# Performance work log

Measured on AMD Instinct MI355X. Metric: run time of the kernel, lower is better.

## Reference

```python
import jax, jax.numpy as jnp
import numpy as np

N_NODES = 50000
N_EDGES = 1600000
DIM = 128
EDGE_DIM = 16
IN_DIM = 2 * DIM + EDGE_DIM


def setup_inputs() -> dict:
    key = jax.random.key(0)
    ks = jax.random.split(key, 8)
    h = jax.random.normal(ks[0], (N_NODES, DIM), dtype=jnp.float32)
    src = jax.random.randint(ks[1], (N_EDGES,), 0, N_NODES)
    dst = jax.random.randint(ks[2], (N_EDGES,), 0, N_NODES)
    edge_attr = jax.random.normal(ks[3], (N_EDGES, EDGE_DIM), dtype=jnp.float32)
    # Linear weights stored as [in, out] so x @ W + b
    W1 = jax.random.normal(ks[4], (IN_DIM, DIM), dtype=jnp.float32) / np.sqrt(IN_DIM)
    b1 = jnp.zeros((DIM,), dtype=jnp.float32)
    W2 = jax.random.normal(ks[5], (DIM, DIM), dtype=jnp.float32) / np.sqrt(DIM)
    b2 = jnp.zeros((DIM,), dtype=jnp.float32)
    gamma = jnp.ones((DIM,), dtype=jnp.float32)
    beta = jnp.zeros((DIM,), dtype=jnp.float32)
    return {"h": h, "src": src, "dst": dst, "edge_attr": edge_attr,
            "W1": W1, "b1": b1, "W2": W2, "b2": b2, "gamma": gamma, "beta": beta}


def _layer_norm(x, gamma, beta, eps=1e-5):
    mu = jnp.mean(x, axis=-1, keepdims=True)
    var = jnp.mean(jnp.square(x - mu), axis=-1, keepdims=True)
    return (x - mu) * jax.lax.rsqrt(var + eps) * gamma + beta


def reference(h, src, dst, edge_attr, W1, b1, W2, b2, gamma, beta):
    # gather endpoint features + edge attrs -> [E, 2*dim+edge_dim]
    x = jnp.concatenate([h[src], h[dst], edge_attr], axis=-1)
    hdn = jax.nn.gelu(x @ W1 + b1, approximate=False)  # torch nn.GELU default is exact
    messages = hdn @ W2 + b2                           # [E, dim]
    # scatter-add messages to destination nodes
    agg = jax.ops.segment_sum(messages, dst, num_segments=h.shape[0])
    return _layer_norm(h + agg, gamma, beta)
```

## Files before the change

kernel.cpp:

```cpp
#include <hip/hip_runtime.h>
#include <math.h>

#define NUM_NODES 50000
#define NUM_EDGES 1600000
#define DIM 128
#define EDGE_DIM 16
#define NKT1 18
#define NKT2 8
#define MT 64
#define CSTRIDE 132
#define NSCAN 196
#define NODE_BLOCKS ((NUM_NODES + 63) / 64)

typedef short bf16x8 __attribute__((ext_vector_type(8)));
typedef float floatx16 __attribute__((ext_vector_type(16)));
typedef unsigned short ushort4v __attribute__((ext_vector_type(4)));
typedef unsigned short ushort8v __attribute__((ext_vector_type(8)));

__device__ __forceinline__ unsigned short f2b(float f) {
    unsigned u = __builtin_bit_cast(unsigned, f);
    u += 0x7FFFu + ((u >> 16) & 1u);
    return (unsigned short)(u >> 16);
}

__global__ void setup_kernel(const float* __restrict__ W1, const float* __restrict__ W2,
                             short* __restrict__ W1f, short* __restrict__ W2f,
                             const float* __restrict__ h, unsigned short* __restrict__ h_bf,
                             const int* __restrict__ dst, int* __restrict__ counts)
{
    int b = blockIdx.x, tid = threadIdx.x;
    if (b < 26) {
        int gid = b * 256 + tid;
        if (gid < NKT1 * 4 * 64) {
            int lane = gid & 63, nb = (gid >> 6) & 3, kt = gid >> 8;
            int n = nb * 32 + (lane & 31);
            int kbase = kt * 16 + (lane >> 5) * 8;
            #pragma unroll
            for (int j = 0; j < 8; ++j) {
                int k = kbase + j;
                W1f[gid * 8 + j] = (k < 272) ? (short)f2b(W1[(size_t)k * DIM + n]) : (short)0;
            }
        } else if (gid < NKT1 * 4 * 64 + NKT2 * 4 * 64) {
            int g2 = gid - NKT1 * 4 * 64;
            int lane = g2 & 63, nb = (g2 >> 6) & 3, kt = g2 >> 8;
            int n = nb * 32 + (lane & 31);
            int kbase = kt * 16 + (lane >> 5) * 8;
            #pragma unroll
            for (int j = 0; j < 8; ++j)
                W2f[g2 * 8 + j] = (short)f2b(W2[(size_t)(kbase + j) * DIM + n]);
        }
    } else if (b < 6276) {
        int t = (b - 26) * 256 + tid;
        float4 v = ((const float4*)h)[t];
        ushort4v o;
        o.x = f2b(v.x); o.y = f2b(v.y); o.z = f2b(v.z); o.w = f2b(v.w);
        ((ushort4v*)h_bf)[t] = o;
    } else {
        int e = (b - 6276) * 256 + tid;
        atomicAdd(&counts[dst[e]], 1);
    }
}

__global__ void scanA_kernel(const int* __restrict__ counts, int* __restrict__ bsum) {
    __shared__ int sb[256];
    int t = threadIdx.x, i = blockIdx.x * 256 + t;
    int v = (i < NUM_NODES) ? counts[i] : 0;
    sb[t] = v; __syncthreads();
    for (int off = 1; off < 256; off <<= 1) {
        int x = (t >= off) ? sb[t - off] : 0;
        __syncthreads(); sb[t] += x; __syncthreads();
    }
    if (t == 255) bsum[blockIdx.x] = sb[255];
}

__global__ void scanB_kernel(const int* __restrict__ bsum, int* __restrict__ boffs) {
    __shared__ int sb[256];
    int t = threadIdx.x;
    int v = (t < NSCAN) ? bsum[t] : 0;
    sb[t] = v; __syncthreads();
    for (int off = 1; off < 256; off <<= 1) {
        int x = (t >= off) ? sb[t - off] : 0;
        __syncthreads(); sb[t] += x; __syncthreads();
    }
    if (t < NSCAN) boffs[t] = sb[t] - v;
}

__global__ void scanC_kernel(const int* __restrict__ counts, const int* __restrict__ boffs,
                             int* __restrict__ cursor) {
    __shared__ int sb[256];
    int t = threadIdx.x, i = blockIdx.x * 256 + t;
    int v = (i < NUM_NODES) ? counts[i] : 0;
    sb[t] = v; __syncthreads();
    for (int off = 1; off < 256; off <<= 1) {
        int x = (t >= off) ? sb[t - off] : 0;
        __syncthreads(); sb[t] += x; __syncthreads();
    }
    if (i < NUM_NODES) cursor[i] = boffs[blockIdx.x] + sb[t] - v;
}

__global__ void scatter_kernel(const int* __restrict__ src, const int* __restrict__ dst,
                               int* __restrict__ cursor, int2* __restrict__ se_s)
{
    int e = blockIdx.x * 256 + threadIdx.x;
    int d = dst[e];
    int p = atomicAdd(&cursor[d], 1);
    se_s[p] = make_int2(src[e] | (d << 16), e);
}

__global__ __launch_bounds__(256, 4) void edge_kernel(
    const unsigned short* __restrict__ h_bf,
    const int2* __restrict__ se_s, const float* __restrict__ ea,
    const short* __restrict__ W1f, const float* __restrict__ pb1,
    float* __restrict__ aggh)
{
    __shared__ __align__(16) short xbuf[36 * 64 * 8];
    __shared__ int dstl[MT];
    float* cbuf = (float*)xbuf;
    float* pbuf = (float*)xbuf;

    const int tid = threadIdx.x;
    const int lane = tid & 63, wave = tid >> 6;
    const long long base = (long long)blockIdx.x * MT;

    {
        int row = lane;
        int2 se = se_s[base + row];
        int sn = se.x & 0xFFFF;
        int dn = ((unsigned)se.x) >> 16;
        if (tid < MT) dstl[tid] = dn;
        const ushort8v* hs = (const ushort8v*)(h_bf + (size_t)sn * DIM);
        const ushort8v* hd = (const ushort8v*)(h_bf + (size_t)dn * DIM);
        #pragma unroll
        for (int it = 0; it < 4; ++it) {
            int kt2 = it * 4 + wave;
            *(ushort8v*)&xbuf[(kt2 * 64 + row) * 8] = hs[kt2];
        }
        #pragma unroll
        for (int it = 0; it < 4; ++it) {
            int kt2 = it * 4 + wave;
            *(ushort8v*)&xbuf[((16 + kt2) * 64 + row) * 8] = hd[kt2];
        }
        if (tid < 128) {
            int r2 = tid >> 1, hc = tid & 1;
            int eid = se_s[base + r2].y;
            const float4* er = (const float4*)(ea + (size_t)eid * EDGE_DIM + hc * 8);
            float4 v0 = er[0], v1 = er[1];
            ushort8v o;
            o[0] = f2b(v0.x); o[1] = f2b(v0.y); o[2] = f2b(v0.z); o[3] = f2b(v0.w);
            o[4] = f2b(v1.x); o[5] = f2b(v1.y); o[6] = f2b(v1.z); o[7] = f2b(v1.w);
            *(ushort8v*)&xbuf[((32 + hc) * 64 + r2) * 8] = o;
        } else {
            int t2 = tid - 128;
            int r2 = t2 >> 1, hc = t2 & 1;
            ushort8v z = {0, 0, 0, 0, 0, 0, 0, 0};
            *(ushort8v*)&xbuf[((34 + hc) * 64 + r2) * 8] = z;
        }
    }
    __syncthreads();

    const int lm = lane & 31, half = lane >> 5;

    floatx16 acc0 = {}, acc1 = {};
    #pragma unroll
    for (int kt = 0; kt < NKT1; ++kt) {
        bf16x8 a0 = *(const bf16x8*)&xbuf[((kt * 2 + half) * 64 + lm) * 8];
        bf16x8 a1 = *(const bf16x8*)&xbuf[((kt * 2 + half) * 64 + 32 + lm) * 8];
        bf16x8 b  = *(const bf16x8*)(W1f + ((kt * 4 + wave) * 64 + lane) * 8);
        acc0 = __builtin_amdgcn_mfma_f32_32x32x16_bf16(a0, b, acc0, 0, 0, 0);
        acc1 = __builtin_amdgcn_mfma_f32_32x32x16_bf16(a1, b, acc1, 0, 0, 0);
    }
    __syncthreads();

    {
        float bb = pb1[wave * 32 + lm];
        #pragma unroll
        for (int s = 0; s < 2; ++s) {
            const floatx16& A = s ? acc1 : acc0;
            #pragma unroll
            for (int r = 0; r < 16; ++r) {
                int rr = (r & 3) + 8 * (r >> 2) + 4 * half;
                float v = A[r] + bb;
                float u = v * (1.5957691216f + 0.0713548163f * v * v);
                u = fminf(u, 80.f);
                float t = __expf(u);
                float g = v * t * __builtin_amdgcn_rcpf(t + 1.f);
                cbuf[(s * 32 + rr) * CSTRIDE + wave * 32 + lm] = g;
            }
        }
    }
    __syncthreads();

    int q = tid & 31, g = tid >> 5;
    float4 s4;
    {
        int r0 = g * 8;
        float4 v[8];
        #pragma unroll
        for (int r = 0; r < 8; ++r)
            v[r] = *(const float4*)&cbuf[(r0 + r) * CSTRIDE + q * 4];
        int d[8];
        #pragma unroll
        for (int r = 0; r < 8; ++r) d[r] = dstl[r0 + r];
        s4 = make_float4(0.f, 0.f, 0.f, 0.f);
        int cur = d[0];
        #pragma unroll
        for (int r = 0; r < 8; ++r) {
            s4.x += v[r].x; s4.y += v[r].y; s4.z += v[r].z; s4.w += v[r].w;
            if (r < 7 && d[r + 1] != cur) {
                float* ap = &aggh[(size_t)cur * DIM + q * 4];
                atomicAdd(ap + 0, s4.x); atomicAdd(ap + 1, s4.y);
                atomicAdd(ap + 2, s4.z); atomicAdd(ap + 3, s4.w);
                s4 = make_float4(0.f, 0.f, 0.f, 0.f);
                cur = d[r + 1];
            }
        }
    }
    __syncthreads();
    *(float4*)&pbuf[g * CSTRIDE + q * 4] = s4;
    __syncthreads();

    if (tid < 128) {
        int col = tid;
        float p[8];
        #pragma unroll
        for (int gg = 0; gg < 8; ++gg) p[gg] = pbuf[gg * CSTRIDE + col];
        int t[8];
        #pragma unroll
        for (int gg = 0; gg < 8; ++gg) t[gg] = dstl[gg * 8 + 7];
        float s = 0.f;
        int cur = t[0];
        #pragma unroll
        for (int gg = 0; gg < 8; ++gg) {
            s += p[gg];
            int nxt = (gg == 7) ? -1 : t[gg + 1];
            if (nxt != cur) {
                atomicAdd(&aggh[(size_t)cur * DIM + col], s);
                s = 0.f;
                cur = nxt;
            }
        }
    }
}

__global__ __launch_bounds__(256, 4) void node_ln_kernel(
    const float* __restrict__ aggh, const int* __restrict__ counts,
    const short* __restrict__ W2f, const float* __restrict__ pb2,
    const float* __restrict__ h, const float* __restrict__ gamma,
    const float* __restrict__ beta, float* __restrict__ out)
{
    __shared__ __align__(16) float sbuf[64 * CSTRIDE];
    __shared__ int cntl[64];
    short* abuf = (short*)sbuf;

    const int tid = threadIdx.x;
    const int n0 = blockIdx.x * 64;

    if (tid < 64) {
        int node = n0 + tid;
        cntl[tid] = (node < NUM_NODES) ? counts[node] : 0;
    }
    #pragma unroll
    for (int it = 0; it < 4; ++it) {
        int g = it * 256 + tid;
        int kt2 = g >> 6, row = g & 63;
        int node = n0 + row;
        ushort8v o = {0, 0, 0, 0, 0, 0, 0, 0};
        if (node < NUM_NODES) {
            const float4* p = (const float4*)(aggh + (size_t)node * DIM + kt2 * 8);
            float4 v0 = p[0], v1 = p[1];
            o[0] = f2b(v0.x); o[1] = f2b(v0.y); o[2] = f2b(v0.z); o[3] = f2b(v0.w);
            o[4] = f2b(v1.x); o[5] = f2b(v1.y); o[6] = f2b(v1.z); o[7] = f2b(v1.w);
        }
        *(ushort8v*)&abuf[(kt2 * 64 + row) * 8] = o;
    }
    __syncthreads();

    const int lane = tid & 63, wave = tid >> 6;
    const int lm = lane & 31, half = lane >> 5;

    floatx16 acc0 = {}, acc1 = {};
    #pragma unroll
    for (int kt = 0; kt < NKT2; ++kt) {
        bf16x8 a0 = *(const bf16x8*)&abuf[((kt * 2 + half) * 64 + lm) * 8];
        bf16x8 a1 = *(const bf16x8*)&abuf[((kt * 2 + half) * 64 + 32 + lm) * 8];
        bf16x8 b  = *(const bf16x8*)(W2f + ((kt * 4 + wave) * 64 + lane) * 8);
        acc0 = __builtin_amdgcn_mfma_f32_32x32x16_bf16(a0, b, acc0, 0, 0, 0);
        acc1 = __builtin_amdgcn_mfma_f32_32x32x16_bf16(a1, b, acc1, 0, 0, 0);
    }
    __syncthreads();

    float bb2 = pb2[wave * 32 + lm];
    #pragma unroll
    for (int s = 0; s < 2; ++s) {
        const floatx16& A = s ? acc1 : acc0;
        #pragma unroll
        for (int r = 0; r < 16; ++r) {
            int rr = (r & 3) + 8 * (r >> 2) + 4 * half;
            int row = s * 32 + rr;
            sbuf[row * CSTRIDE + wave * 32 + lm] = A[r] + (float)cntl[row] * bb2;
        }
    }
    __syncthreads();

    {
        int row = tid >> 2, q = tid & 3;
        int node = n0 + row;
        if (node < NUM_NODES) {
            float4 xv[8];
            float s = 0.f, ss = 0.f;
            const float4* hp = (const float4*)(h + (size_t)node * DIM + q * 32);
            #pragma unroll
            for (int i = 0; i < 8; ++i) {
                float4 c = *(const float4*)&sbuf[row * CSTRIDE + q * 32 + i * 4];
                float4 hh = hp[i];
                float4 x;
                x.x = c.x + hh.x; x.y = c.y + hh.y; x.z = c.z + hh.z; x.w = c.w + hh.w;
                xv[i] = x;
                s  += x.x + x.y + x.z + x.w;
                ss += x.x * x.x + x.y * x.y + x.z * x.z + x.w * x.w;
            }
            s  += __shfl_xor(s, 1, 64);  s  += __shfl_xor(s, 2, 64);
            ss += __shfl_xor(ss, 1, 64); ss += __shfl_xor(ss, 2, 64);
            float mu = s * (1.f / DIM);
            float var = ss * (1.f / DIM) - mu * mu;
            float rs = rsqrtf(var + 1e-5f);
            const float4* gp = (const float4*)(gamma + q * 32);
            const float4* bp = (const float4*)(beta + q * 32);
            float4* op = (float4*)(out + (size_t)node * DIM + q * 32);
            #pragma unroll
            for (int i = 0; i < 8; ++i) {
                float4 g4 = gp[i], b4 = bp[i], o;
                o.x = (xv[i].x - mu) * rs * g4.x + b4.x;
                o.y = (xv[i].y - mu) * rs * g4.y + b4.y;
                o.z = (xv[i].z - mu) * rs * g4.z + b4.z;
                o.w = (xv[i].w - mu) * rs * g4.w + b4.w;
                op[i] = o;
            }
        }
    }
}

extern "C" void kernel_launch(void* const* d_in, const int* in_sizes, int n_in,
                              void* d_out, int out_size, void* d_ws, size_t ws_size,
                              hipStream_t stream)
{
    const float* h     = (const float*)d_in[0];
    const int*   src   = (const int*)d_in[1];
    const int*   dst   = (const int*)d_in[2];
    const float* ea    = (const float*)d_in[3];
    const float* W1    = (const float*)d_in[4];
    const float* pb1   = (const float*)d_in[5];
    const float* W2    = (const float*)d_in[6];
    const float* pb2   = (const float*)d_in[7];
    const float* gamma = (const float*)d_in[8];
    const float* beta  = (const float*)d_in[9];
    float* out = (float*)d_out;

    char* ws = (char*)d_ws;
    short* W1f   = (short*)ws;
    short* W2f   = (short*)(ws + 73728);
    int* counts  = (int*)(ws + 106496);
    int* cursor  = (int*)(ws + 306496);
    int* bsum    = (int*)(ws + 506496);
    int* boffs   = (int*)(ws + 507520);
    int2* se_s   = (int2*)(ws + 508544);
    unsigned short* h_bf = (unsigned short*)(ws + 19708544);
    float* aggh  = (float*)(ws + 32508544);

    hipMemsetAsync(counts, 0, NUM_NODES * sizeof(int), stream);
    hipMemsetAsync(aggh, 0, (size_t)NUM_NODES * DIM * sizeof(float), stream);

    setup_kernel<<<12526, 256, 0, stream>>>(W1, W2, W1f, W2f, h, h_bf, dst, counts);
    scanA_kernel<<<NSCAN, 256, 0, stream>>>(counts, bsum);
    scanB_kernel<<<1, 256, 0, stream>>>(bsum, boffs);
    scanC_kernel<<<NSCAN, 256, 0, stream>>>(counts, boffs, cursor);
    scatter_kernel<<<NUM_EDGES / 256, 256, 0, stream>>>(src, dst, cursor, se_s);
    edge_kernel<<<NUM_EDGES / MT, 256, 0, stream>>>(h_bf, se_s, ea, W1f, pb1, aggh);
    node_ln_kernel<<<NODE_BLOCKS, 256, 0, stream>>>(aggh, counts, W2f, pb2,
                                                    h, gamma, beta, out);
}
```

Before: 619.4 us.

## Fuse prep, scan and scatter into one cooperative kernel with grid syncs

Replaces two memsets and five small launches (setup, three scan stages, scatter) with a single cooperative kernel of 1024 blocks that uses grid-wide syncs between phases. The goal is to remove launch overhead and inter-kernel gaps in the preprocessing pipeline. The counting-sort scatter now uses a non-temporal 64-bit store. The trade-offs are five grid barriers, grid-stride loops over fewer threads, and a co-residency requirement for the cooperative launch.

```diff
diff --git a/kernel.cpp b/kernel.cpp
--- a/kernel.cpp
+++ b/kernel.cpp
@@ -1,5 +1,8 @@
 #include <hip/hip_runtime.h>
+#include <hip/hip_cooperative_groups.h>
 #include <math.h>
+
+namespace cg = cooperative_groups;
 
 #define NUM_NODES 50000
 #define NUM_EDGES 1600000
@@ -11,6 +14,7 @@
 #define CSTRIDE 132
 #define NSCAN 196
 #define NODE_BLOCKS ((NUM_NODES + 63) / 64)
+#define COOP_BLOCKS 1024
 
 typedef short bf16x8 __attribute__((ext_vector_type(8)));
 typedef float floatx16 __attribute__((ext_vector_type(16)));
@@ -23,88 +27,92 @@
     return (unsigned short)(u >> 16);
 }
 
-__global__ void setup_kernel(const float* __restrict__ W1, const float* __restrict__ W2,
-                             short* __restrict__ W1f, short* __restrict__ W2f,
-                             const float* __restrict__ h, unsigned short* __restrict__ h_bf,
-                             const int* __restrict__ dst, int* __restrict__ counts)
+__global__ __launch_bounds__(256, 8) void prep_all_kernel(
+    const float* __restrict__ W1, const float* __restrict__ W2,
+    short* __restrict__ W1f, short* __restrict__ W2f,
+    const float* __restrict__ h, unsigned short* __restrict__ h_bf,
+    const int* __restrict__ src, const int* __restrict__ dst,
+    int* __restrict__ counts, int* __restrict__ bsum, int* __restrict__ boffs,
+    int* __restrict__ cursor, int2* __restrict__ se_s, float* __restrict__ aggh)
 {
-    int b = blockIdx.x, tid = threadIdx.x;
-    if (b < 26) {
-        int gid = b * 256 + tid;
-        if (gid < NKT1 * 4 * 64) {
-            int lane = gid & 63, nb = (gid >> 6) & 3, kt = gid >> 8;
-            int n = nb * 32 + (lane & 31);
-            int kbase = kt * 16 + (lane >> 5) * 8;
-            #pragma unroll
-            for (int j = 0; j < 8; ++j) {
-                int k = kbase + j;
-                W1f[gid * 8 + j] = (k < 272) ? (short)f2b(W1[(size_t)k * DIM + n]) : (short)0;
-            }
-        } else if (gid < NKT1 * 4 * 64 + NKT2 * 4 * 64) {
-            int g2 = gid - NKT1 * 4 * 64;
-            int lane = g2 & 63, nb = (g2 >> 6) & 3, kt = g2 >> 8;
-            int n = nb * 32 + (lane & 31);
-            int kbase = kt * 16 + (lane >> 5) * 8;
-            #pragma unroll
-            for (int j = 0; j < 8; ++j)
-                W2f[g2 * 8 + j] = (short)f2b(W2[(size_t)(kbase + j) * DIM + n]);
-        }
-    } else if (b < 6276) {
-        int t = (b - 26) * 256 + tid;
-        float4 v = ((const float4*)h)[t];
+    cg::grid_group grid = cg::this_grid();
+    __shared__ int sb[256];
+    const int tid = threadIdx.x;
+    const int gstride = COOP_BLOCKS * 256;
+    const int gid0 = blockIdx.x * 256 + tid;
+
+    for (int i = gid0; i < NUM_NODES; i += gstride) counts[i] = 0;
+    for (int i = gid0; i < NUM_NODES * (DIM / 4); i += gstride)
+        ((float4*)aggh)[i] = make_float4(0.f, 0.f, 0.f, 0.f);
+    grid.sync();
+
+    if (gid0 < NKT1 * 4 * 64) {
+        int gid = gid0;
+        int lane = gid & 63, nb = (gid >> 6) & 3, kt = gid >> 8;
+        int n = nb * 32 + (lane & 31);
+        int kbase = kt * 16 + (lane >> 5) * 8;
+        #pragma unroll
+        for (int j = 0; j < 8; ++j) {
+            int k = kbase + j;
+            W1f[gid * 8 + j] = (k < 272) ? (short)f2b(W1[(size_t)k * DIM + n]) : (short)0;
+        }
+    } else if (gid0 < NKT1 * 4 * 64 + NKT2 * 4 * 64) {
+        int g2 = gid0 - NKT1 * 4 * 64;
+        int lane = g2 & 63, nb = (g2 >> 6) & 3, kt = g2 >> 8;
+        int n = nb * 32 + (lane & 31);
+        int kbase = kt * 16 + (lane >> 5) * 8;
+        #pragma unroll
+        for (int j = 0; j < 8; ++j)
+            W2f[g2 * 8 + j] = (short)f2b(W2[(size_t)(kbase + j) * DIM + n]);
+    }
+    for (int i = gid0; i < (NUM_NODES * DIM) / 4; i += gstride) {
+        float4 v = ((const float4*)h)[i];
         ushort4v o;
         o.x = f2b(v.x); o.y = f2b(v.y); o.z = f2b(v.z); o.w = f2b(v.w);
-        ((ushort4v*)h_bf)[t] = o;
-    } else {
-        int e = (b - 6276) * 256 + tid;
+        ((ushort4v*)h_bf)[i] = o;
+    }
+    for (int e = gid0; e < NUM_EDGES; e += gstride)
         atomicAdd(&counts[dst[e]], 1);
-    }
-}
-
-__global__ void scanA_kernel(const int* __restrict__ counts, int* __restrict__ bsum) {
-    __shared__ int sb[256];
-    int t = threadIdx.x, i = blockIdx.x * 256 + t;
-    int v = (i < NUM_NODES) ? counts[i] : 0;
-    sb[t] = v; __syncthreads();
-    for (int off = 1; off < 256; off <<= 1) {
-        int x = (t >= off) ? sb[t - off] : 0;
-        __syncthreads(); sb[t] += x; __syncthreads();
-    }
-    if (t == 255) bsum[blockIdx.x] = sb[255];
-}
-
-__global__ void scanB_kernel(const int* __restrict__ bsum, int* __restrict__ boffs) {
-    __shared__ int sb[256];
-    int t = threadIdx.x;
-    int v = (t < NSCAN) ? bsum[t] : 0;
-    sb[t] = v; __syncthreads();
-    for (int off = 1; off < 256; off <<= 1) {
-        int x = (t >= off) ? sb[t - off] : 0;
-        __syncthreads(); sb[t] += x; __syncthreads();
-    }
-    if (t < NSCAN) boffs[t] = sb[t] - v;
-}
-
-__global__ void scanC_kernel(const int* __restrict__ counts, const int* __restrict__ boffs,
-                             int* __restrict__ cursor) {
-    __shared__ int sb[256];
-    int t = threadIdx.x, i = blockIdx.x * 256 + t;
-    int v = (i < NUM_NODES) ? counts[i] : 0;
-    sb[t] = v; __syncthreads();
-    for (int off = 1; off < 256; off <<= 1) {
-        int x = (t >= off) ? sb[t - off] : 0;
-        __syncthreads(); sb[t] += x; __syncthreads();
-    }
-    if (i < NUM_NODES) cursor[i] = boffs[blockIdx.x] + sb[t] - v;
-}
-
-__global__ void scatter_kernel(const int* __restrict__ src, const int* __restrict__ dst,
-                               int* __restrict__ cursor, int2* __restrict__ se_s)
-{
-    int e = blockIdx.x * 256 + threadIdx.x;
-    int d = dst[e];
-    int p = atomicAdd(&cursor[d], 1);
-    se_s[p] = make_int2(src[e] | (d << 16), e);
+    grid.sync();
+
+    if (blockIdx.x < NSCAN) {
+        int i = blockIdx.x * 256 + tid;
+        int v = (i < NUM_NODES) ? counts[i] : 0;
+        sb[tid] = v; __syncthreads();
+        for (int off = 1; off < 256; off <<= 1) {
+            int x = (tid >= off) ? sb[tid - off] : 0;
+            __syncthreads(); sb[tid] += x; __syncthreads();
+        }
+        if (tid == 255) bsum[blockIdx.x] = sb[255];
+        if (i < NUM_NODES) cursor[i] = sb[tid] - v;
+    }
+    grid.sync();
+
+    if (blockIdx.x == 0) {
+        int v = (tid < NSCAN) ? bsum[tid] : 0;
+        sb[tid] = v; __syncthreads();
+        for (int off = 1; off < 256; off <<= 1) {
+            int x = (tid >= off) ? sb[tid - off] : 0;
+            __syncthreads(); sb[tid] += x; __syncthreads();
+        }
+        if (tid < NSCAN) boffs[tid] = sb[tid] - v;
+    }
+    grid.sync();
+
+    if (blockIdx.x < NSCAN) {
+        int i = blockIdx.x * 256 + tid;
+        if (i < NUM_NODES) cursor[i] += boffs[blockIdx.x];
+    }
+    grid.sync();
+
+    for (int e = gid0; e < NUM_EDGES; e += gstride) {
+        int d = dst[e];
+        int p = atomicAdd(&cursor[d], 1);
+        unsigned lo = (unsigned)(src[e] | (d << 16));
+        long long packed = (long long)((unsigned long long)lo |
+                                       ((unsigned long long)(unsigned)e << 32));
+        __builtin_nontemporal_store(packed, (long long*)&se_s[p]);
+    }
 }
 
 __global__ __launch_bounds__(256, 4) void edge_kernel(
@@ -367,14 +375,14 @@
     unsigned short* h_bf = (unsigned short*)(ws + 19708544);
     float* aggh  = (float*)(ws + 32508544);
 
-    hipMemsetAsync(counts, 0, NUM_NODES * sizeof(int), stream);
-    hipMemsetAsync(aggh, 0, (size_t)NUM_NODES * DIM * sizeof(float), stream);
-
-    setup_kernel<<<12526, 256, 0, stream>>>(W1, W2, W1f, W2f, h, h_bf, dst, counts);
-    scanA_kernel<<<NSCAN, 256, 0, stream>>>(counts, bsum);
-    scanB_kernel<<<1, 256, 0, stream>>>(bsum, boffs);
-    scanC_kernel<<<NSCAN, 256, 0, stream>>>(counts, boffs, cursor);
-    scatter_kernel<<<NUM_EDGES / 256, 256, 0, stream>>>(src, dst, cursor, se_s);
+    void* cargs[] = {
+        (void*)&W1, (void*)&W2, (void*)&W1f, (void*)&W2f,
+        (void*)&h, (void*)&h_bf, (void*)&src, (void*)&dst,
+        (void*)&counts, (void*)&bsum, (void*)&boffs,
+        (void*)&cursor, (void*)&se_s, (void*)&aggh
+    };
+    hipLaunchCooperativeKernel((const void*)prep_all_kernel,
+                               dim3(COOP_BLOCKS), dim3(256), cargs, 0, stream);
     edge_kernel<<<NUM_EDGES / MT, 256, 0, stream>>>(h_bf, se_s, ea, W1f, pb1, aggh);
     node_ln_kernel<<<NODE_BLOCKS, 256, 0, stream>>>(aggh, counts, W2f, pb2,
                                                     h, gamma, beta, out);
```

Result: slower. 1.154 ms (+86.4%).

## Merge scan passes, fold accumulator zeroing into setup, drop padded K tile

Applied to the files above, without the earlier changes.

Merges the block-offset scan and the final cursor scan into one kernel, where each block reduces the preceding block sums itself. This removes one launch and one dependent step. The accumulator memset moves into the setup kernel as extra blocks. The first GEMM now uses 17 K-tiles instead of 18 because 272 is an exact multiple of 16, which drops the zero-padding tile, its LDS writes and one MFMA pair per tile. Each scan block now does a redundant small reduction over bsum.

```diff
diff --git a/kernel.cpp b/kernel.cpp
--- a/kernel.cpp
+++ b/kernel.cpp
@@ -5,13 +5,18 @@
 #define NUM_EDGES 1600000
 #define DIM 128
 #define EDGE_DIM 16
-#define NKT1 18
+#define NKT1 17
 #define NKT2 8
 #define MT 64
 #define CSTRIDE 132
 #define NSCAN 196
 #define NODE_BLOCKS ((NUM_NODES + 63) / 64)
 
+#define SB_W     25
+#define SB_HCONV (SB_W + 6250)
+#define SB_HIST  (SB_HCONV + 6250)
+#define SB_ZERO  (SB_HIST + 1563)
+
 typedef short bf16x8 __attribute__((ext_vector_type(8)));
 typedef float floatx16 __attribute__((ext_vector_type(16)));
 typedef unsigned short ushort4v __attribute__((ext_vector_type(4)));
@@ -26,20 +31,19 @@
 __global__ void setup_kernel(const float* __restrict__ W1, const float* __restrict__ W2,
                              short* __restrict__ W1f, short* __restrict__ W2f,
                              const float* __restrict__ h, unsigned short* __restrict__ h_bf,
-                             const int* __restrict__ dst, int* __restrict__ counts)
+                             const int* __restrict__ dst, int* __restrict__ counts,
+                             float* __restrict__ aggh)
 {
     int b = blockIdx.x, tid = threadIdx.x;
-    if (b < 26) {
+    if (b < SB_W) {
         int gid = b * 256 + tid;
         if (gid < NKT1 * 4 * 64) {
             int lane = gid & 63, nb = (gid >> 6) & 3, kt = gid >> 8;
             int n = nb * 32 + (lane & 31);
             int kbase = kt * 16 + (lane >> 5) * 8;
             #pragma unroll
-            for (int j = 0; j < 8; ++j) {
-                int k = kbase + j;
-                W1f[gid * 8 + j] = (k < 272) ? (short)f2b(W1[(size_t)k * DIM + n]) : (short)0;
-            }
+            for (int j = 0; j < 8; ++j)
+                W1f[gid * 8 + j] = (short)f2b(W1[(size_t)(kbase + j) * DIM + n]);
         } else if (gid < NKT1 * 4 * 64 + NKT2 * 4 * 64) {
             int g2 = gid - NKT1 * 4 * 64;
             int lane = g2 & 63, nb = (g2 >> 6) & 3, kt = g2 >> 8;
@@ -49,15 +53,21 @@
             for (int j = 0; j < 8; ++j)
                 W2f[g2 * 8 + j] = (short)f2b(W2[(size_t)(kbase + j) * DIM + n]);
         }
-    } else if (b < 6276) {
-        int t = (b - 26) * 256 + tid;
+    } else if (b < SB_HCONV) {
+        int t = (b - SB_W) * 256 + tid;
         float4 v = ((const float4*)h)[t];
         ushort4v o;
         o.x = f2b(v.x); o.y = f2b(v.y); o.z = f2b(v.z); o.w = f2b(v.w);
         ((ushort4v*)h_bf)[t] = o;
+    } else if (b < SB_HIST) {
+        int e = (b - SB_HCONV) * 256 + tid;
+        atomicAdd(&counts[dst[e]], 1);
     } else {
-        int e = (b - 6276) * 256 + tid;
-        atomicAdd(&counts[dst[e]], 1);
+        int i0 = ((b - SB_HIST) * 256 + tid) * 4;
+        float4 z = make_float4(0.f, 0.f, 0.f, 0.f);
+        #pragma unroll
+        for (int j = 0; j < 4; ++j)
+            if (i0 + j < NUM_NODES * (DIM / 4)) ((float4*)aggh)[i0 + j] = z;
     }
 }
 
@@ -73,29 +83,25 @@
     if (t == 255) bsum[blockIdx.x] = sb[255];
 }
 
-__global__ void scanB_kernel(const int* __restrict__ bsum, int* __restrict__ boffs) {
+__global__ void scanBC_kernel(const int* __restrict__ counts, const int* __restrict__ bsum,
+                              int* __restrict__ cursor) {
     __shared__ int sb[256];
-    int t = threadIdx.x;
-    int v = (t < NSCAN) ? bsum[t] : 0;
-    sb[t] = v; __syncthreads();
-    for (int off = 1; off < 256; off <<= 1) {
-        int x = (t >= off) ? sb[t - off] : 0;
-        __syncthreads(); sb[t] += x; __syncthreads();
-    }
-    if (t < NSCAN) boffs[t] = sb[t] - v;
-}
-
-__global__ void scanC_kernel(const int* __restrict__ counts, const int* __restrict__ boffs,
-                             int* __restrict__ cursor) {
-    __shared__ int sb[256];
-    int t = threadIdx.x, i = blockIdx.x * 256 + t;
+    int t = threadIdx.x, b = blockIdx.x, i = b * 256 + t;
     int v = (i < NUM_NODES) ? counts[i] : 0;
     sb[t] = v; __syncthreads();
     for (int off = 1; off < 256; off <<= 1) {
         int x = (t >= off) ? sb[t - off] : 0;
         __syncthreads(); sb[t] += x; __syncthreads();
     }
-    if (i < NUM_NODES) cursor[i] = boffs[blockIdx.x] + sb[t] - v;
+    int myexcl = sb[t] - v;
+    __syncthreads();
+    sb[t] = (t < b && t < NSCAN) ? bsum[t] : 0;
+    __syncthreads();
+    for (int off = 128; off > 0; off >>= 1) {
+        if (t < off) sb[t] += sb[t + off];
+        __syncthreads();
+    }
+    if (i < NUM_NODES) cursor[i] = sb[0] + myexcl;
 }
 
 __global__ void scatter_kernel(const int* __restrict__ src, const int* __restrict__ dst,
@@ -113,7 +119,7 @@
     const short* __restrict__ W1f, const float* __restrict__ pb1,
     float* __restrict__ aggh)
 {
-    __shared__ __align__(16) short xbuf[36 * 64 * 8];
+    __shared__ __align__(16) short xbuf[34 * 64 * 8];
     __shared__ int dstl[MT];
     float* cbuf = (float*)xbuf;
     float* pbuf = (float*)xbuf;
@@ -149,11 +155,6 @@
             o[0] = f2b(v0.x); o[1] = f2b(v0.y); o[2] = f2b(v0.z); o[3] = f2b(v0.w);
             o[4] = f2b(v1.x); o[5] = f2b(v1.y); o[6] = f2b(v1.z); o[7] = f2b(v1.w);
             *(ushort8v*)&xbuf[((32 + hc) * 64 + r2) * 8] = o;
-        } else {
-            int t2 = tid - 128;
-            int r2 = t2 >> 1, hc = t2 & 1;
-            ushort8v z = {0, 0, 0, 0, 0, 0, 0, 0};
-            *(ushort8v*)&xbuf[((34 + hc) * 64 + r2) * 8] = z;
         }
     }
     __syncthreads();
@@ -358,22 +359,19 @@
 
     char* ws = (char*)d_ws;
     short* W1f   = (short*)ws;
-    short* W2f   = (short*)(ws + 73728);
-    int* counts  = (int*)(ws + 106496);
-    int* cursor  = (int*)(ws + 306496);
-    int* bsum    = (int*)(ws + 506496);
-    int* boffs   = (int*)(ws + 507520);
-    int2* se_s   = (int2*)(ws + 508544);
-    unsigned short* h_bf = (unsigned short*)(ws + 19708544);
-    float* aggh  = (float*)(ws + 32508544);
+    short* W2f   = (short*)(ws + 69632);
+    int* counts  = (int*)(ws + 102400);
+    int* cursor  = (int*)(ws + 302400);
+    int* bsum    = (int*)(ws + 502400);
+    int2* se_s   = (int2*)(ws + 503424);
+    unsigned short* h_bf = (unsigned short*)(ws + 13303424);
+    float* aggh  = (float*)(ws + 26103424);
 
     hipMemsetAsync(counts, 0, NUM_NODES * sizeof(int), stream);
-    hipMemsetAsync(aggh, 0, (size_t)NUM_NODES * DIM * sizeof(float), stream);
-
-    setup_kernel<<<12526, 256, 0, stream>>>(W1, W2, W1f, W2f, h, h_bf, dst, counts);
+    setup_kernel<<<SB_ZERO, 256, 0, stream>>>(W1, W2, W1f, W2f, h, h_bf, dst,
+                                              counts, aggh);
     scanA_kernel<<<NSCAN, 256, 0, stream>>>(counts, bsum);
-    scanB_kernel<<<1, 256, 0, stream>>>(bsum, boffs);
-    scanC_kernel<<<NSCAN, 256, 0, stream>>>(counts, boffs, cursor);
+    scanBC_kernel<<<NSCAN, 256, 0, stream>>>(counts, bsum, cursor);
     scatter_kernel<<<NUM_EDGES / 256, 256, 0, stream>>>(src, dst, cursor, se_s);
     edge_kernel<<<NUM_EDGES / MT, 256, 0, stream>>>(h_bf, se_s, ea, W1f, pb1, aggh);
     node_ln_kernel<<<NODE_BLOCKS, 256, 0, stream>>>(aggh, counts, W2f, pb2,
```

After: 618.8 us. No clear change (-0.1%).
